# Kernel tuning notes

Measured on AMD Instinct MI355X. Metric: run time of the kernel, lower is better.

The kernel has to match this reference:

```python
import jax, jax.numpy as jnp
import numpy as np

DEPTH = 5

def _path_table(depth):
    # For each leaf, ancestor internal-node index and right/left direction at each of `depth` steps.
    n_internal = 2 ** depth - 1
    n_leaves = 2 ** depth
    anc = np.zeros((n_leaves, depth), dtype=np.int32)
    is_right = np.zeros((n_leaves, depth), dtype=bool)
    for leaf in range(n_leaves):
        node = leaf + n_internal
        for d in range(depth):
            parent = (node - 1) // 2
            anc[leaf, d] = parent
            is_right[leaf, d] = (node % 2 == 0)
            node = parent
    return anc, is_right


def setup_inputs() -> dict:
    key = jax.random.key(0)
    k1, k2, k3 = jax.random.split(key, 3)
    B, F, T = 131072, 128, 20
    n_internal = 2 ** DEPTH - 1
    n_leaves = 2 ** DEPTH
    x = jax.random.normal(k1, (B, F), dtype=jnp.float32)
    split_weights = jax.random.normal(k2, (T, n_internal, F), dtype=jnp.float32) * 0.1
    split_bias = jnp.zeros((T, n_internal), dtype=jnp.float32)
    leaf_logits = jax.random.normal(k3, (T, n_leaves, 2), dtype=jnp.float32) * 0.1
    tree_weights = jnp.ones((T,), dtype=jnp.float32) / T
    # feature masks: fraction 0.7 of features active per tree
    rng = np.random.default_rng(0)
    n_feat_per_tree = max(1, int(F * 0.7))
    masks = np.zeros((T, F), dtype=np.float32)
    for t in range(T):
        idx = rng.permutation(F)[:n_feat_per_tree]
        masks[t, idx] = 1.0
    feature_masks = jnp.asarray(masks)
    return {"x": x, "split_weights": split_weights, "split_bias": split_bias,
            "leaf_logits": leaf_logits, "tree_weights": tree_weights,
            "feature_masks": feature_masks}


def reference(x, split_weights, split_bias, leaf_logits, tree_weights, feature_masks):
    T, N, F = split_weights.shape
    anc, is_right = _path_table(DEPTH)  # static numpy tables [L, DEPTH]
    # Fuse feature masking into the split weights (avoids materializing [T,B,F]).
    Wm = split_weights * feature_masks[:, None, :]           # [T,N,F]
    logits = jnp.einsum('bf,tnf->tbn', x, Wm) + split_bias[:, None, :]
    sp = jax.nn.sigmoid(logits)                              # [T,B,N], temperature = 1.0
    L = N + 1
    leaf_probs = jnp.ones(sp.shape[:2] + (L,), dtype=sp.dtype)  # [T,B,L]
    for d in range(DEPTH):  # small static loop over tree depth
        g = sp[:, :, anc[:, d]]                              # [T,B,L]
        leaf_probs = leaf_probs * jnp.where(is_right[None, None, :, d], g, 1.0 - g)
    leaf_class_probs = jax.nn.softmax(leaf_logits, axis=-1)  # [T,L,2]
    tree_out = jnp.einsum('tbl,tlc->tbc', leaf_probs, leaf_class_probs)
    w = jax.nn.softmax(tree_weights)                         # [T]
    return jnp.einsum('t,tbc->bc', w, tree_out)
```

## Files before the change

### kernel.cpp

```cpp
#include <hip/hip_runtime.h>

typedef __attribute__((ext_vector_type(8))) short bf16x8;
typedef __attribute__((ext_vector_type(4))) float floatx4;

#define T_TREES 20
#define N_NODES 32
#define F_DIM 128
#define M_TILE 128
#define S_SP 36

#define NLOG2E 1.4426950408889634f

__device__ __forceinline__ short f2bf(float f) {
    unsigned u = __float_as_uint(f);
    u += 0x7fffu + ((u >> 16) & 1u);
    return (short)(u >> 16);
}
__device__ __forceinline__ float bf2f(short h) {
    return __uint_as_float(((unsigned)(unsigned short)h) << 16);
}

__device__ __forceinline__ float sig_from_scaled(float u) {
    return __builtin_amdgcn_rcpf(1.f + __builtin_amdgcn_exp2f(u));
}

__global__ void nrf_prep(const float* __restrict__ sw, const float* __restrict__ sb,
                         const float* __restrict__ ll, const float* __restrict__ tw,
                         const float* __restrict__ fm,
                         short* __restrict__ w_all, float* __restrict__ bias_p,
                         float* __restrict__ lv0) {
    int t = blockIdx.x, slice = blockIdx.y, tid = threadIdx.x;

    const float* fmt = fm + t * F_DIM;
    const float* swt = sw + t * 31 * F_DIM;
    int idx = slice * 512 + tid;
    #pragma unroll
    for (int r = 0; r < 2; ++r, idx += 256) {
        int n = idx >> 7, f = idx & 127;
        short wb = (n < 31 && fmt[f] != 0.f) ? f2bf(swt[n * F_DIM + f]) : (short)0;
        w_all[t * (N_NODES * F_DIM) + idx] = wb;
    }

    if (slice == 0) {
        __shared__ float tws[T_TREES];
        if (tid < T_TREES) tws[tid] = tw[tid];
        __syncthreads();
        if (tid < N_NODES) {
            float m = -1e30f;
            for (int i = 0; i < T_TREES; ++i) m = fmaxf(m, bf2f(f2bf(tws[i])));
            float s = 0.f;
            for (int i = 0; i < T_TREES; ++i) s += __expf(bf2f(f2bf(tws[i])) - m);
            float wt = __expf(bf2f(f2bf(tws[t])) - m) / s;

            float bv = (tid < 31) ? bf2f(f2bf(sb[t * 31 + tid])) : 0.f;
            bias_p[t * N_NODES + tid] = bv * (-NLOG2E);
            float a  = bf2f(f2bf(ll[(t * 32 + tid) * 2 + 0]));
            float bb = bf2f(f2bf(ll[(t * 32 + tid) * 2 + 1]));
            float mx = fmaxf(a, bb);
            float e0 = __expf(a - mx), e1 = __expf(bb - mx);
            lv0[t * N_NODES + tid] = wt * e0 / (e0 + e1);
        }
    }
}

__global__ __launch_bounds__(256, 4) void nrf_main(const float* __restrict__ x,
        const short* __restrict__ w_all, const float* __restrict__ bias_p,
        const float* __restrict__ lv0, float* __restrict__ out) {
    __shared__ short bstage[N_NODES * F_DIM];
    __shared__ float sp_all[4][N_NODES * S_SP];
    __shared__ float lv_s[T_TREES * N_NODES];
    __shared__ float bias_s[T_TREES * N_NODES];

    int tid = threadIdx.x;
    int wave = tid >> 6, lane = tid & 63;
    int q = lane >> 4, c16 = lane & 15;

    for (int i = tid; i < T_TREES * N_NODES; i += 256) { lv_s[i] = lv0[i]; bias_s[i] = bias_p[i]; }

    float* spb = sp_all[wave];
    int rowBase = blockIdx.x * M_TILE + wave * 32;

    bf16x8 afrag[2][4];
    #pragma unroll
    for (int mi = 0; mi < 2; ++mi) {
        const float* xr = x + (size_t)(rowBase + mi * 16 + c16) * F_DIM;
        #pragma unroll
        for (int ks = 0; ks < 4; ++ks) {
            const float4* p = (const float4*)(xr + ks * 32 + q * 8);
            float4 f0 = p[0], f1 = p[1];
            bf16x8 v;
            v[0]=f2bf(f0.x); v[1]=f2bf(f0.y); v[2]=f2bf(f0.z); v[3]=f2bf(f0.w);
            v[4]=f2bf(f1.x); v[5]=f2bf(f1.y); v[6]=f2bf(f1.z); v[7]=f2bf(f1.w);
            afrag[mi][ks] = v;
        }
    }

    const unsigned soff0 = (unsigned)(tid * 32) ^ ((unsigned)((tid >> 3) & 7) << 4);
    const bf16x8* wsrc = (const bf16x8*)w_all + tid * 2;

    {
        bf16x8 s0 = wsrc[0], s1 = wsrc[1];
        *(bf16x8*)((char*)bstage + soff0) = s0;
        *(bf16x8*)((char*)bstage + (soff0 ^ 16u)) = s1;
    }

    int s = lane & 15, h = lane >> 4;
    int s_node = 3 + h;
    float acc0 = 0.f, acc1 = 0.f;
    __syncthreads();

    #pragma unroll
    for (int t = 0; t < T_TREES; ++t) {
        bf16x8 pf0, pf1;
        if (t + 1 < T_TREES) {
            const bf16x8* src = (const bf16x8*)(w_all + (t + 1) * (N_NODES * F_DIM)) + tid * 2;
            pf0 = src[0]; pf1 = src[1];
        }

        bf16x8 bfrag[2][4];
        const char* bb = (const char*)bstage;
        #pragma unroll
        for (int ni = 0; ni < 2; ++ni) {
            unsigned row = (unsigned)(ni * 16 + c16);
            unsigned swz = (row & 7u) << 4;
            #pragma unroll
            for (int ks = 0; ks < 4; ++ks) {
                unsigned lin = row * 256u + (unsigned)(ks * 64 + q * 16);
                bfrag[ni][ks] = *(const bf16x8*)(bb + (lin ^ swz));
            }
        }
        __syncthreads();

        floatx4 acc[2][2];
        #pragma unroll
        for (int mi = 0; mi < 2; ++mi)
            #pragma unroll
            for (int ni = 0; ni < 2; ++ni)
                acc[mi][ni] = (floatx4){0.f,0.f,0.f,0.f};
        #pragma unroll
        for (int ks = 0; ks < 4; ++ks)
            #pragma unroll
            for (int mi = 0; mi < 2; ++mi)
                #pragma unroll
                for (int ni = 0; ni < 2; ++ni)
                    acc[mi][ni] = __builtin_amdgcn_mfma_f32_16x16x32_bf16(
                        afrag[mi][ks], bfrag[ni][ks], acc[mi][ni], 0, 0, 0);

        #pragma unroll
        for (int ni = 0; ni < 2; ++ni) {
            int col = ni * 16 + c16;
            float bv = bias_s[t * N_NODES + col];
            #pragma unroll
            for (int mi = 0; mi < 2; ++mi) {
                float4 v;
                v.x = sig_from_scaled(fmaf(acc[mi][ni][0], -NLOG2E, bv));
                v.y = sig_from_scaled(fmaf(acc[mi][ni][1], -NLOG2E, bv));
                v.z = sig_from_scaled(fmaf(acc[mi][ni][2], -NLOG2E, bv));
                v.w = sig_from_scaled(fmaf(acc[mi][ni][3], -NLOG2E, bv));
                *(float4*)&spb[col * S_SP + mi * 16 + q * 4] = v;
            }
        }
        float g0a = spb[s],                          g0b = spb[s + 16];
        int n1 = 1 + (h >> 1);
        float g1a = spb[n1 * S_SP + s],              g1b = spb[n1 * S_SP + s + 16];
        float g2a = spb[s_node * S_SP + s],          g2b = spb[s_node * S_SP + s + 16];
        int n3a = 2 * s_node + 1, n3b = 2 * s_node + 2;
        float g3aa = spb[n3a * S_SP + s],            g3ab = spb[n3a * S_SP + s + 16];
        float g3ba = spb[n3b * S_SP + s],            g3bb = spb[n3b * S_SP + s + 16];
        int n4 = 4 * s_node + 3;
        float g4aa = spb[n4 * S_SP + s],             g4ab = spb[n4 * S_SP + s + 16];
        float g4ba = spb[(n4+1) * S_SP + s],         g4bb = spb[(n4+1) * S_SP + s + 16];
        float g4ca = spb[(n4+2) * S_SP + s],         g4cb = spb[(n4+2) * S_SP + s + 16];
        float g4da = spb[(n4+3) * S_SP + s],         g4db = spb[(n4+3) * S_SP + s + 16];

        const float* lvt = &lv_s[t * N_NODES + h * 8];

        {
            float f0 = (h & 2) ? g0a : 1.f - g0a;
            float f1 = (h & 1) ? g1a : 1.f - g1a;
            float pre = f0 * f1;
            float p1 = pre * g2a, p0 = pre - p1;
            float q1 = p0 * g3aa, q0 = p0 - q1;
            float q3 = p1 * g3ba, q2 = p1 - q3;
            float r1 = q0 * g4aa, r0 = q0 - r1;
            float r3 = q1 * g4ba, r2 = q1 - r3;
            float r5 = q2 * g4ca, r4 = q2 - r5;
            float r7 = q3 * g4da, r6 = q3 - r7;
            acc0 += r0*lvt[0] + r1*lvt[1] + r2*lvt[2] + r3*lvt[3]
                  + r4*lvt[4] + r5*lvt[5] + r6*lvt[6] + r7*lvt[7];
        }
        {
            float f0 = (h & 2) ? g0b : 1.f - g0b;
            float f1 = (h & 1) ? g1b : 1.f - g1b;
            float pre = f0 * f1;
            float p1 = pre * g2b, p0 = pre - p1;
            float q1 = p0 * g3ab, q0 = p0 - q1;
            float q3 = p1 * g3bb, q2 = p1 - q3;
            float r1 = q0 * g4ab, r0 = q0 - r1;
            float r3 = q1 * g4bb, r2 = q1 - r3;
            float r5 = q2 * g4cb, r4 = q2 - r5;
            float r7 = q3 * g4db, r6 = q3 - r7;
            acc1 += r0*lvt[0] + r1*lvt[1] + r2*lvt[2] + r3*lvt[3]
                  + r4*lvt[4] + r5*lvt[5] + r6*lvt[6] + r7*lvt[7];
        }

        if (t + 1 < T_TREES) {
            *(bf16x8*)((char*)bstage + soff0) = pf0;
            *(bf16x8*)((char*)bstage + (soff0 ^ 16u)) = pf1;
            __syncthreads();
        }
    }

    acc0 += __shfl_xor(acc0, 16, 64);
    acc0 += __shfl_xor(acc0, 32, 64);
    acc1 += __shfl_xor(acc1, 16, 64);
    acc1 += __shfl_xor(acc1, 32, 64);
    if (h == 0) {
        float2 o0; o0.x = acc0; o0.y = 1.f - acc0;
        *(float2*)(out + (size_t)(rowBase + s) * 2) = o0;
        float2 o1; o1.x = acc1; o1.y = 1.f - acc1;
        *(float2*)(out + (size_t)(rowBase + 16 + s) * 2) = o1;
    }
}

extern "C" void kernel_launch(void* const* d_in, const int* in_sizes, int n_in,
                              void* d_out, int out_size, void* d_ws, size_t ws_size,
                              hipStream_t stream) {
    const float* x  = (const float*)d_in[0];
    const float* sw = (const float*)d_in[1];
    const float* sb = (const float*)d_in[2];
    const float* ll = (const float*)d_in[3];
    const float* tw = (const float*)d_in[4];
    const float* fm = (const float*)d_in[5];
    float* out = (float*)d_out;

    short* w_all  = (short*)d_ws;
    float* bias_p = (float*)((char*)d_ws + 163840);
    float* lv0    = (float*)((char*)d_ws + 166400);

    dim3 pgrid(T_TREES, 8);
    nrf_prep<<<pgrid, 256, 0, stream>>>(sw, sb, ll, tw, fm, w_all, bias_p, lv0);

    int B = in_sizes[0] / F_DIM;
    nrf_main<<<B / M_TILE, 256, 0, stream>>>(x, w_all, bias_p, lv0, out);
}
```

Measured before the change: 143.2 us.

## Double-buffer tree weights and software-pipeline MFMA one tree ahead

Adds a second LDS staging buffer for the per-tree split weights and restructures the tree loop so the MFMA for tree t+1 is issued before the sigmoid and leaf-probability work of tree t. Global prefetch now runs two trees ahead, and one barrier per iteration replaces the previous two. This is meant to overlap matrix-core work with the VALU/LDS path math and remove a barrier. In exchange it costs an extra 8 KB of LDS and keeps a second set of accumulators live, which may hurt occupancy under launch_bounds(256,4).

```diff
diff --git a/kernel.cpp b/kernel.cpp
--- a/kernel.cpp
+++ b/kernel.cpp
@@ -66,7 +66,7 @@
 __global__ __launch_bounds__(256, 4) void nrf_main(const float* __restrict__ x,
         const short* __restrict__ w_all, const float* __restrict__ bias_p,
         const float* __restrict__ lv0, float* __restrict__ out) {
-    __shared__ short bstage[N_NODES * F_DIM];
+    __shared__ short bstage[2][N_NODES * F_DIM];
     __shared__ float sp_all[4][N_NODES * S_SP];
     __shared__ float lv_s[T_TREES * N_NODES];
     __shared__ float bias_s[T_TREES * N_NODES];
@@ -96,12 +96,15 @@
     }
 
     const unsigned soff0 = (unsigned)(tid * 32) ^ ((unsigned)((tid >> 3) & 7) << 4);
-    const bf16x8* wsrc = (const bf16x8*)w_all + tid * 2;
 
     {
-        bf16x8 s0 = wsrc[0], s1 = wsrc[1];
-        *(bf16x8*)((char*)bstage + soff0) = s0;
-        *(bf16x8*)((char*)bstage + (soff0 ^ 16u)) = s1;
+        const bf16x8* s0p = (const bf16x8*)w_all + tid * 2;
+        const bf16x8* s1p = (const bf16x8*)(w_all + N_NODES * F_DIM) + tid * 2;
+        bf16x8 a0 = s0p[0], a1 = s0p[1], b0 = s1p[0], b1 = s1p[1];
+        *(bf16x8*)((char*)bstage[0] + soff0) = a0;
+        *(bf16x8*)((char*)bstage[0] + (soff0 ^ 16u)) = a1;
+        *(bf16x8*)((char*)bstage[1] + soff0) = b0;
+        *(bf16x8*)((char*)bstage[1] + (soff0 ^ 16u)) = b1;
     }
 
     int s = lane & 15, h = lane >> 4;
@@ -109,16 +112,11 @@
     float acc0 = 0.f, acc1 = 0.f;
     __syncthreads();
 
-    #pragma unroll
-    for (int t = 0; t < T_TREES; ++t) {
-        bf16x8 pf0, pf1;
-        if (t + 1 < T_TREES) {
-            const bf16x8* src = (const bf16x8*)(w_all + (t + 1) * (N_NODES * F_DIM)) + tid * 2;
-            pf0 = src[0]; pf1 = src[1];
-        }
-
+    floatx4 accP[2][2][2];
+
+    {
         bf16x8 bfrag[2][4];
-        const char* bb = (const char*)bstage;
+        const char* bb = (const char*)bstage[0];
         #pragma unroll
         for (int ni = 0; ni < 2; ++ni) {
             unsigned row = (unsigned)(ni * 16 + c16);
@@ -129,22 +127,57 @@
                 bfrag[ni][ks] = *(const bf16x8*)(bb + (lin ^ swz));
             }
         }
-        __syncthreads();
-
-        floatx4 acc[2][2];
         #pragma unroll
         for (int mi = 0; mi < 2; ++mi)
             #pragma unroll
             for (int ni = 0; ni < 2; ++ni)
-                acc[mi][ni] = (floatx4){0.f,0.f,0.f,0.f};
+                accP[0][mi][ni] = (floatx4){0.f,0.f,0.f,0.f};
         #pragma unroll
         for (int ks = 0; ks < 4; ++ks)
             #pragma unroll
             for (int mi = 0; mi < 2; ++mi)
                 #pragma unroll
                 for (int ni = 0; ni < 2; ++ni)
-                    acc[mi][ni] = __builtin_amdgcn_mfma_f32_16x16x32_bf16(
-                        afrag[mi][ks], bfrag[ni][ks], acc[mi][ni], 0, 0, 0);
+                    accP[0][mi][ni] = __builtin_amdgcn_mfma_f32_16x16x32_bf16(
+                        afrag[mi][ks], bfrag[ni][ks], accP[0][mi][ni], 0, 0, 0);
+    }
+    __syncthreads();
+
+    #pragma unroll
+    for (int t = 0; t < T_TREES; ++t) {
+        const int p = t & 1, pn = p ^ 1;
+        bf16x8 pf0, pf1;
+        if (t + 2 < T_TREES) {
+            const bf16x8* src = (const bf16x8*)(w_all + (t + 2) * (N_NODES * F_DIM)) + tid * 2;
+            pf0 = src[0]; pf1 = src[1];
+        }
+        if (t + 1 < T_TREES) {
+            bf16x8 bfrag[2][4];
+            const char* bb = (const char*)bstage[pn];
+            #pragma unroll
+            for (int ni = 0; ni < 2; ++ni) {
+                unsigned row = (unsigned)(ni * 16 + c16);
+                unsigned swz = (row & 7u) << 4;
+                #pragma unroll
+                for (int ks = 0; ks < 4; ++ks) {
+                    unsigned lin = row * 256u + (unsigned)(ks * 64 + q * 16);
+                    bfrag[ni][ks] = *(const bf16x8*)(bb + (lin ^ swz));
+                }
+            }
+            #pragma unroll
+            for (int mi = 0; mi < 2; ++mi)
+                #pragma unroll
+                for (int ni = 0; ni < 2; ++ni)
+                    accP[pn][mi][ni] = (floatx4){0.f,0.f,0.f,0.f};
+            #pragma unroll
+            for (int ks = 0; ks < 4; ++ks)
+                #pragma unroll
+                for (int mi = 0; mi < 2; ++mi)
+                    #pragma unroll
+                    for (int ni = 0; ni < 2; ++ni)
+                        accP[pn][mi][ni] = __builtin_amdgcn_mfma_f32_16x16x32_bf16(
+                            afrag[mi][ks], bfrag[ni][ks], accP[pn][mi][ni], 0, 0, 0);
+        }
 
         #pragma unroll
         for (int ni = 0; ni < 2; ++ni) {
@@ -153,10 +186,10 @@
             #pragma unroll
             for (int mi = 0; mi < 2; ++mi) {
                 float4 v;
-                v.x = sig_from_scaled(fmaf(acc[mi][ni][0], -NLOG2E, bv));
-                v.y = sig_from_scaled(fmaf(acc[mi][ni][1], -NLOG2E, bv));
-                v.z = sig_from_scaled(fmaf(acc[mi][ni][2], -NLOG2E, bv));
-                v.w = sig_from_scaled(fmaf(acc[mi][ni][3], -NLOG2E, bv));
+                v.x = sig_from_scaled(fmaf(accP[p][mi][ni][0], -NLOG2E, bv));
+                v.y = sig_from_scaled(fmaf(accP[p][mi][ni][1], -NLOG2E, bv));
+                v.z = sig_from_scaled(fmaf(accP[p][mi][ni][2], -NLOG2E, bv));
+                v.w = sig_from_scaled(fmaf(accP[p][mi][ni][3], -NLOG2E, bv));
                 *(float4*)&spb[col * S_SP + mi * 16 + q * 4] = v;
             }
         }
@@ -204,11 +237,11 @@
                   + r4*lvt[4] + r5*lvt[5] + r6*lvt[6] + r7*lvt[7];
         }
 
-        if (t + 1 < T_TREES) {
-            *(bf16x8*)((char*)bstage + soff0) = pf0;
-            *(bf16x8*)((char*)bstage + (soff0 ^ 16u)) = pf1;
-            __syncthreads();
-        }
+        if (t + 2 < T_TREES) {
+            *(bf16x8*)((char*)bstage[p] + soff0) = pf0;
+            *(bf16x8*)((char*)bstage[p] + (soff0 ^ 16u)) = pf1;
+        }
+        __syncthreads();
     }
 
     acc0 += __shfl_xor(acc0, 16, 64);
```

Result: no change. 141.3 us (-1.4%).
